# Kernel tuning notes

Measured on AMD Instinct MI355X. Metric: run time of the kernel, lower is better.

Reference implementation:

```python
import jax, jax.numpy as jnp
import numpy as np

# Bernstein-basis theta coefficients for d=2 (calculate_theta2(2)),
# inv_coeff order: [x^0, x^1, x^2]
THETAS = ((3.0, -3.0, 0.75), (0.0, 3.0, -1.5), (0.0, 0.0, 0.75))
HIGH_ORDER = 2

N_NODES = 50000
N_EDGES = 800000
IN_DIM, HID_DIM, OUT_DIM = 128, 64, 2


def setup_inputs() -> dict:
    key = jax.random.key(0)
    ks = jax.random.split(key, 16)
    f32 = jnp.float32
    def w(k, shape, fan_in):
        return jax.random.normal(k, shape, dtype=f32) * (1.0 / np.sqrt(fan_in))
    return {
        "in_feat": jax.random.normal(ks[0], (N_NODES, IN_DIM), dtype=f32),
        "src": jax.random.randint(ks[1], (N_EDGES,), 0, N_NODES, dtype=jnp.int32),
        "dst": jax.random.randint(ks[2], (N_EDGES,), 0, N_NODES, dtype=jnp.int32),
        "W1": w(ks[3], (IN_DIM, HID_DIM), IN_DIM), "b1": jnp.zeros((HID_DIM,), f32),
        "W2": w(ks[4], (HID_DIM, HID_DIM), HID_DIM), "b2": jnp.zeros((HID_DIM,), f32),
        "W3": w(ks[5], (HID_DIM * 5, HID_DIM), HID_DIM * 5), "b3": jnp.zeros((HID_DIM,), f32),
        "W4": w(ks[6], (HID_DIM, OUT_DIM), HID_DIM), "b4": jnp.zeros((OUT_DIM,), f32),
        "Wg1": w(ks[7], (IN_DIM, HID_DIM), IN_DIM), "bg1": jnp.zeros((HID_DIM,), f32),
        "Wg2": w(ks[8], (HID_DIM, IN_DIM), HID_DIM), "bg2": jnp.zeros((IN_DIM,), f32),
    }


def _spmm(x, src, dst, n):
    # y[v] = sum_{(u,v) in E} x[u]   (DGL update_all(copy_u, sum))
    return jax.ops.segment_sum(x[src], dst, num_segments=n)


def reference(in_feat, src, dst, W1, b1, W2, b2, W3, b3, W4, b4, Wg1, bg1, Wg2, bg2):
    n = in_feat.shape[0]
    ones_e = jnp.ones(src.shape[0], dtype=in_feat.dtype)
    deg_in = jnp.clip(jax.ops.segment_sum(ones_e, dst, num_segments=n), 1.0)
    deg_out = jnp.clip(jax.ops.segment_sum(ones_e, src, num_segments=n), 1.0)
    din = (deg_in ** -0.5)[:, None]   # [N,1]
    dout = (deg_out ** -0.5)[:, None]

    def lap(f):
        # f - D^{-1/2} A D^{-1/2} f  (in-degree norm, as in unnLaplacian)
        return f - _spmm(f * din, src, dst, n) * din

    # MLP front-end
    h = jax.nn.relu(in_feat @ W1 + b1)
    h = jax.nn.relu(h @ W2 + b2)

    branches = []
    # BandConv branches (lin=False): theta-weighted Laplacian polynomial
    for theta in THETAS:
        f = h
        acc = theta[0] * h
        for k in range(1, len(theta)):
            f = lap(f)
            acc = acc + theta[k] * f
        branches.append(acc)
    # HighConv branches: repeated Laplacian, num_layer = 1..HIGH_ORDER
    f = h
    for j in range(HIGH_ORDER):
        f = lap(f)
        branches.append(f)

    h_final = jnp.concatenate(branches, axis=-1)  # [N, 5*hid]
    out = jax.nn.relu(h_final @ W3 + b3) @ W4 + b4  # [N, out_dim]

    # GCN branch on self-loop-free graph (same edges here): symmetric norm GraphConv
    def gconv(x, W, b):
        return _spmm(x * dout, src, dst, n) * din @ W + b
    emb = gconv(jax.nn.relu(gconv(in_feat, Wg1, bg1)), Wg2, bg2)  # [N, in_dim]

    return out, emb
```

## Files before the change

kernel.cpp:

```cpp
#include <hip/hip_runtime.h>
#include <hip/hip_bf16.h>
#include <math.h>

#define NN 50000
#define NE 800000
#define C64 64
#define CE 12500
#define RW2 6250
#define NW 25000
#define HISTB 256
#define RB 98
#define GB 782
#define ZSB 782
#define FSG 3125
#define FSB 6250

typedef _Float16 half8 __attribute__((ext_vector_type(8)));
typedef _Float16 half4v __attribute__((ext_vector_type(4)));
typedef float f32x4 __attribute__((ext_vector_type(4)));
typedef unsigned short ushort4v __attribute__((ext_vector_type(4)));

static inline int cdiv(int a, int b) { return (a + b - 1) / b; }


__device__ inline size_t pack_pos(int k, int n, int K, int M) {
    int tile = n >> 4;
    int kstep = k >> 5;
    int quad = (k >> 3) & 3;
    int j = k & 7;
    int lane = (quad << 4) | (n & 15);
    return ((size_t)(tile * (K >> 5) + kstep) * 64 + lane) * 8 + j;
}

__device__ void pack_std_dev(int bx, const float* __restrict__ W, _Float16* __restrict__ Wpk,
                             int K, int M) {
    int idx = bx * 256 + threadIdx.x;
    if (idx >= K * M) return;
    int k = idx / M, n = idx % M;
    Wpk[pack_pos(k, n, K, M)] = (_Float16)W[idx];
}

__device__ void pack_wc_dev(int bx, const float* __restrict__ W3, _Float16* __restrict__ wcpk) {
    int idx = bx * 256 + threadIdx.x;
    if (idx >= 3 * 4096) return;
    int b = idx >> 12;
    int rem = idx & 4095;
    int k = rem >> 6, n = rem & 63;
    float w0 = W3[(0 * 64 + k) * 64 + n];
    float w1 = W3[(1 * 64 + k) * 64 + n];
    float w2 = W3[(2 * 64 + k) * 64 + n];
    float w3 = W3[(3 * 64 + k) * 64 + n];
    float w4 = W3[(4 * 64 + k) * 64 + n];
    float v;
    if (b == 0)      v = 3.f * w0;
    else if (b == 1) v = -3.f * w0 + 3.f * w1 + w3;
    else             v = 0.75f * w0 - 1.5f * w1 + 0.75f * w2 + w4;
    wcpk[pack_pos(b * 64 + k, n, 192, 64)] = (_Float16)v;
}

__launch_bounds__(256)
__global__ void k_init(const float* __restrict__ W1, _Float16* __restrict__ W1pk,
                       const float* __restrict__ W2, _Float16* __restrict__ W2pk,
                       const float* __restrict__ Wg1, _Float16* __restrict__ Wg1pk,
                       const float* __restrict__ Wg2, _Float16* __restrict__ Wg2pk,
                       const float* __restrict__ W3, _Float16* __restrict__ wcpk) {
    int bx = blockIdx.x;
    if (bx < 32) { pack_std_dev(bx, W1, W1pk, 128, 64); return; }
    bx -= 32;
    if (bx < 16) { pack_std_dev(bx, W2, W2pk, 64, 64); return; }
    bx -= 16;
    if (bx < 32) { pack_std_dev(bx, Wg1, Wg1pk, 128, 64); return; }
    bx -= 32;
    if (bx < 32) { pack_std_dev(bx, Wg2, Wg2pk, 64, 128); return; }
    bx -= 32;
    pack_wc_dev(bx, W3, wcpk);
}


__device__ void hist_dev(int bx, const int* __restrict__ idx, unsigned* __restrict__ H,
                         unsigned* __restrict__ cnt) {
    int c = bx & 63, r = bx >> 6;
    int tid = threadIdx.x;
    for (int j = tid; j < RW2; j += 256) cnt[j] = 0;
    __syncthreads();
    int lo = r * 12500;
    const int* p = idx + c * CE;
    for (int i = tid; i < CE; i += 256) {
        int v = p[i] - lo;
        if ((unsigned)v < 12500u)
            atomicAdd(&cnt[v >> 1], 1u << ((v & 1) * 16));
    }
    __syncthreads();
    unsigned* outp = H + (size_t)c * NW + r * RW2;
    for (int j = tid; j < RW2; j += 256) outp[j] = cnt[j];
}

__device__ void reduce_dev(int bx, const unsigned* __restrict__ H, int* __restrict__ dgo,
                           float* __restrict__ o_rsq, float* __restrict__ o_inv,
                           float* __restrict__ o_sq) {
    int w = bx * 256 + threadIdx.x;
    if (w >= NW) return;
    unsigned slo = 0, shi = 0;
#pragma unroll 8
    for (int c = 0; c < 64; c++) {
        unsigned h = H[(size_t)c * NW + w];
        slo += h & 0xffffu; shi += h >> 16;
    }
    if (dgo) {
        dgo[2 * w]     = slo > 64u ? 64 : (int)slo;
        dgo[2 * w + 1] = shi > 64u ? 64 : (int)shi;
    }
    float f0 = (float)(slo < 1u ? 1u : slo);
    float f1 = (float)(shi < 1u ? 1u : shi);
    o_rsq[2 * w] = rsqrtf(f0); o_rsq[2 * w + 1] = rsqrtf(f1);
    if (o_inv) { o_inv[2 * w] = 1.f / f0; o_inv[2 * w + 1] = 1.f / f1; }
    if (o_sq)  { o_sq[2 * w] = sqrtf(f0); o_sq[2 * w + 1] = sqrtf(f1); }
}

__device__ void prefix_dev(int bx, const unsigned* __restrict__ HD, unsigned* __restrict__ baseD) {
    int w = bx * 256 + threadIdx.x;
    if (w >= NW) return;
    unsigned slo = 0, shi = 0;
    for (int c = 0; c < 64; c++) {
        unsigned b0 = slo > 64u ? 64u : slo;
        unsigned b1 = shi > 64u ? 64u : shi;
        baseD[(size_t)c * NW + w] = b0 | (b1 << 16);
        unsigned h = HD[(size_t)c * NW + w];
        slo += h & 0xffffu; shi += h >> 16;
    }
}

__device__ void scatter_dev(int bx, const int* __restrict__ src, const int* __restrict__ dst,
                            const unsigned* __restrict__ baseD,
                            unsigned short* __restrict__ colsPad,
                            unsigned* __restrict__ cnt) {
    int c = bx & 63, r = bx >> 6;
    int tid = threadIdx.x;
    const unsigned* bslice = baseD + (size_t)c * NW + r * RW2;
    for (int j = tid; j < RW2; j += 256) cnt[j] = bslice[j];
    __syncthreads();
    int lo = r * 12500;
    const int* pd = dst + c * CE;
    const int* ps = src + c * CE;
    for (int i = tid; i < CE; i += 256) {
        int v = pd[i];
        int lv = v - lo;
        if ((unsigned)lv < 12500u) {
            int sh = (lv & 1) * 16;
            unsigned old = atomicAdd(&cnt[lv >> 1], 1u << sh);
            unsigned pos = (old >> sh) & 0xffffu;
            if (pos < 64u) colsPad[(size_t)v * 64 + pos] = (unsigned short)ps[i];
        }
    }
}

__device__ void zscale_dev(int bx, half8* __restrict__ zh8, const float* __restrict__ dout, int N) {
    int idx = bx * 256 + threadIdx.x;
    if (idx >= N * 4) return;
    int row = idx >> 2;
    float m = dout[row];
    half8 a = zh8[idx * 2], b = zh8[idx * 2 + 1];
#pragma unroll
    for (int j = 0; j < 8; j++) {
        a[j] = (_Float16)((float)a[j] * m);
        b[j] = (_Float16)((float)b[j] * m);
    }
    zh8[idx * 2] = a; zh8[idx * 2 + 1] = b;
}


struct HSegs { const _Float16* p[3]; int ld[3]; };

template <int M, int K, bool OUTW, bool RSCA>
__device__ void mg_dev(int bx, HSegs A, const half8* __restrict__ Wpk,
                       const float* __restrict__ bias, int relu,
                       float* __restrict__ C,
                       _Float16* __restrict__ Ch0, const float* __restrict__ ms0,
                       const float* __restrict__ rsc,
                       const float* __restrict__ W4, const float* __restrict__ b4,
                       float* __restrict__ outp, int N) {
    constexpr int NT = M / 16;
    constexpr int NKS = K / 32;
    int tid = threadIdx.x;
    int wave = tid >> 6, lane = tid & 63;
    int quad = lane >> 4, m = lane & 15;
    int row0 = bx * 64 + wave * 16;
    int rowA = row0 + m; if (rowA >= N) rowA = N - 1;
    _Float16 hs = (_Float16)1.f;
    if (RSCA) hs = (_Float16)rsc[rowA];
    f32x4 acc[NT];
#pragma unroll
    for (int t = 0; t < NT; t++) acc[t] = (f32x4){0.f, 0.f, 0.f, 0.f};
#pragma unroll
    for (int ks = 0; ks < NKS; ks++) {
        const _Float16* ap = A.p[ks >> 1] + (size_t)rowA * A.ld[ks >> 1] + (ks & 1) * 32 + quad * 8;
        half8 af = *(const half8*)ap;
        if (RSCA) {
#pragma unroll
            for (int j = 0; j < 8; j++) af[j] *= hs;
        }
#pragma unroll
        for (int t = 0; t < NT; t++) {
            half8 bf = Wpk[(t * NKS + ks) * 64 + lane];
            acc[t] = __builtin_amdgcn_mfma_f32_16x16x32_f16(af, bf, acc[t], 0, 0, 0);
        }
    }
    float outv[NT][4];
#pragma unroll
    for (int t = 0; t < NT; t++) {
        float bv = bias ? bias[t * 16 + m] : 0.f;
#pragma unroll
        for (int r = 0; r < 4; r++) {
            float v = acc[t][r] + bv;
            if (relu) v = fmaxf(v, 0.f);
            outv[t][r] = v;
        }
    }
    if (OUTW) {
        float w40[NT], w41[NT];
#pragma unroll
        for (int t = 0; t < NT; t++) {
            w40[t] = W4[(t * 16 + m) * 2];
            w41[t] = W4[(t * 16 + m) * 2 + 1];
        }
#pragma unroll
        for (int r = 0; r < 4; r++) {
            float p0 = 0.f, p1 = 0.f;
#pragma unroll
            for (int t = 0; t < NT; t++) {
                p0 += outv[t][r] * w40[t];
                p1 += outv[t][r] * w41[t];
            }
#pragma unroll
            for (int off = 1; off < 16; off <<= 1) {
                p0 += __shfl_xor(p0, off);
                p1 += __shfl_xor(p1, off);
            }
            int row = row0 + quad * 4 + r;
            if (m == 0 && row < N) {
                outp[(size_t)row * 2 + 0] = p0 + b4[0];
                outp[(size_t)row * 2 + 1] = p1 + b4[1];
            }
        }
    }
    if (C || Ch0) {
#pragma unroll
        for (int r = 0; r < 4; r++) {
            int row = row0 + quad * 4 + r;
            if (row >= N) continue;
            float m0 = (Ch0 && ms0) ? ms0[row] : 1.f;
#pragma unroll
            for (int t = 0; t < NT; t++) {
                size_t off = (size_t)row * M + t * 16 + m;
                if (C)   C[off] = outv[t][r];
                if (Ch0) Ch0[off] = (_Float16)(outv[t][r] * m0);
            }
        }
    }
}

__device__ void a15_dev(int bx, const float* __restrict__ in_feat,
                        const half8* __restrict__ W1pk, const half8* __restrict__ Wg1pk,
                        const float* __restrict__ b1,
                        _Float16* __restrict__ h1h, _Float16* __restrict__ zh, int N) {
    int tid = threadIdx.x;
    int wave = tid >> 6, lane = tid & 63;
    int quad = lane >> 4, m = lane & 15;
    int row0 = bx * 64 + wave * 16;
    int rowA = row0 + m; if (rowA >= N) rowA = N - 1;
    f32x4 acc0[4], acc1[4];
#pragma unroll
    for (int t = 0; t < 4; t++) {
        acc0[t] = (f32x4){0.f, 0.f, 0.f, 0.f};
        acc1[t] = (f32x4){0.f, 0.f, 0.f, 0.f};
    }
#pragma unroll
    for (int ks = 0; ks < 4; ks++) {
        const float* ap = in_feat + (size_t)rowA * 128 + ks * 32 + quad * 8;
        float4 u = *(const float4*)ap;
        float4 v = *(const float4*)(ap + 4);
        half8 af;
        af[0] = (_Float16)u.x; af[1] = (_Float16)u.y; af[2] = (_Float16)u.z; af[3] = (_Float16)u.w;
        af[4] = (_Float16)v.x; af[5] = (_Float16)v.y; af[6] = (_Float16)v.z; af[7] = (_Float16)v.w;
#pragma unroll
        for (int t = 0; t < 4; t++) {
            acc0[t] = __builtin_amdgcn_mfma_f32_16x16x32_f16(af, W1pk[(t * 4 + ks) * 64 + lane], acc0[t], 0, 0, 0);
            acc1[t] = __builtin_amdgcn_mfma_f32_16x16x32_f16(af, Wg1pk[(t * 4 + ks) * 64 + lane], acc1[t], 0, 0, 0);
        }
    }
#pragma unroll
    for (int r = 0; r < 4; r++) {
        int row = row0 + quad * 4 + r;
        if (row >= N) continue;
#pragma unroll
        for (int t = 0; t < 4; t++) {
            float v0 = fmaxf(acc0[t][r] + b1[t * 16 + m], 0.f);
            h1h[(size_t)row * 64 + t * 16 + m] = (_Float16)v0;
            zh[(size_t)row * 64 + t * 16 + m] = (_Float16)acc1[t][r];
        }
    }
}


__launch_bounds__(256)
__global__ void k_L1(const int* __restrict__ src, const int* __restrict__ dst,
                     unsigned* __restrict__ HD, unsigned* __restrict__ HS,
                     const float* __restrict__ in_feat,
                     const half8* __restrict__ W1pk, const half8* __restrict__ Wg1pk,
                     const float* __restrict__ b1,
                     _Float16* __restrict__ h1h, _Float16* __restrict__ zh, int N) {
    __shared__ unsigned cnt[RW2];
    int bx = blockIdx.x;
    if (bx < HISTB) { hist_dev(bx, dst, HD, cnt); return; }
    bx -= HISTB;
    if (bx < HISTB) { hist_dev(bx, src, HS, cnt); return; }
    bx -= HISTB;
    a15_dev(bx, in_feat, W1pk, Wg1pk, b1, h1h, zh, N);
}

__launch_bounds__(256)
__global__ void k_L2(const unsigned* __restrict__ HD, const unsigned* __restrict__ HS,
                     int* __restrict__ degin, float* __restrict__ din,
                     float* __restrict__ din2, float* __restrict__ dsq,
                     float* __restrict__ dout, unsigned* __restrict__ baseD) {
    int bx = blockIdx.x;
    if (bx < RB) { reduce_dev(bx, HD, degin, din, din2, dsq); return; }
    bx -= RB;
    if (bx < RB) { reduce_dev(bx, HS, nullptr, dout, nullptr, nullptr); return; }
    bx -= RB;
    prefix_dev(bx, HD, baseD);
}

__launch_bounds__(256)
__global__ void k_L3(const int* __restrict__ src, const int* __restrict__ dst,
                     const unsigned* __restrict__ baseD, unsigned short* __restrict__ colsPad,
                     const _Float16* __restrict__ h1h, const half8* __restrict__ W2pk,
                     const float* __restrict__ b2, _Float16* __restrict__ u0h,
                     const float* __restrict__ din,
                     half8* __restrict__ zh8, const float* __restrict__ dout, int N) {
    __shared__ unsigned cnt[RW2];
    int bx = blockIdx.x;
    if (bx < HISTB) { scatter_dev(bx, src, dst, baseD, colsPad, cnt); return; }
    bx -= HISTB;
    if (bx < GB) {
        HSegs A;
        A.p[0] = h1h; A.ld[0] = 64;
        A.p[1] = nullptr; A.ld[1] = 0;
        A.p[2] = nullptr; A.ld[2] = 0;
        mg_dev<64, 64, false, false>(bx, A, W2pk, b2, 1, nullptr, u0h, din,
                                     nullptr, nullptr, nullptr, nullptr, N);
        return;
    }
    bx -= GB;
    zscale_dev(bx, zh8, dout, N);
}


struct SpmmP {
    const half4v* xh; const half4v* fsub_h; const float* rowscale; const float* bias;
    half4v* yh0; const float* ms0; int relu;
};

__launch_bounds__(256)
__global__ void k_FS(SpmmP P0, SpmmP P1, const unsigned short* __restrict__ colsPad,
                     const int* __restrict__ deg, int N) {
    int bx = blockIdx.x;
    bool first = bx < FSG;
    SpmmP P = first ? P0 : P1;
    int g = first ? bx : bx - FSG;
    int tid = threadIdx.x;
    int wave = tid >> 6, lane = tid & 63;
    int quad = lane >> 4, c = lane & 15;
    int row = g * 16 + wave * 4 + quad;
    if (row >= N) return;
    int dg = deg[row];
    const unsigned short* cp = colsPad + (size_t)row * 64;
    float ax = 0.f, ay = 0.f, az = 0.f, aw = 0.f;
    int e = 0;
    for (; e + 7 < dg; e += 8) {
        ushort4v sa = *(const ushort4v*)(cp + e);
        ushort4v sb = *(const ushort4v*)(cp + e + 4);
        half4v v0 = P.xh[(size_t)sa.x * 16 + c];
        half4v v1 = P.xh[(size_t)sa.y * 16 + c];
        half4v v2 = P.xh[(size_t)sa.z * 16 + c];
        half4v v3 = P.xh[(size_t)sa.w * 16 + c];
        half4v v4 = P.xh[(size_t)sb.x * 16 + c];
        half4v v5 = P.xh[(size_t)sb.y * 16 + c];
        half4v v6 = P.xh[(size_t)sb.z * 16 + c];
        half4v v7 = P.xh[(size_t)sb.w * 16 + c];
        ax += (float)v0.x + (float)v1.x + (float)v2.x + (float)v3.x
            + (float)v4.x + (float)v5.x + (float)v6.x + (float)v7.x;
        ay += (float)v0.y + (float)v1.y + (float)v2.y + (float)v3.y
            + (float)v4.y + (float)v5.y + (float)v6.y + (float)v7.y;
        az += (float)v0.z + (float)v1.z + (float)v2.z + (float)v3.z
            + (float)v4.z + (float)v5.z + (float)v6.z + (float)v7.z;
        aw += (float)v0.w + (float)v1.w + (float)v2.w + (float)v3.w
            + (float)v4.w + (float)v5.w + (float)v6.w + (float)v7.w;
    }
    for (; e + 3 < dg; e += 4) {
        ushort4v ss = *(const ushort4v*)(cp + e);
        half4v v0 = P.xh[(size_t)ss.x * 16 + c];
        half4v v1 = P.xh[(size_t)ss.y * 16 + c];
        half4v v2 = P.xh[(size_t)ss.z * 16 + c];
        half4v v3 = P.xh[(size_t)ss.w * 16 + c];
        ax += (float)v0.x + (float)v1.x + (float)v2.x + (float)v3.x;
        ay += (float)v0.y + (float)v1.y + (float)v2.y + (float)v3.y;
        az += (float)v0.z + (float)v1.z + (float)v2.z + (float)v3.z;
        aw += (float)v0.w + (float)v1.w + (float)v2.w + (float)v3.w;
    }
    for (; e < dg; e++) {
        int s = cp[e];
        half4v v = P.xh[(size_t)s * 16 + c];
        ax += (float)v.x; ay += (float)v.y; az += (float)v.z; aw += (float)v.w;
    }
    size_t oidx = (size_t)row * 16 + c;
    if (P.fsub_h) {
        float d = P.rowscale[row];
        half4v f = P.fsub_h[oidx];
        ax = (float)f.x - ax * d; ay = (float)f.y - ay * d;
        az = (float)f.z - az * d; aw = (float)f.w - aw * d;
    } else {
        if (P.rowscale) { float d = P.rowscale[row]; ax *= d; ay *= d; az *= d; aw *= d; }
        if (P.bias) {
            float4 bb = ((const float4*)P.bias)[c];
            ax += bb.x; ay += bb.y; az += bb.z; aw += bb.w;
        }
        if (P.relu) {
            ax = fmaxf(ax, 0.f); ay = fmaxf(ay, 0.f);
            az = fmaxf(az, 0.f); aw = fmaxf(aw, 0.f);
        }
    }
    float mm = P.ms0 ? P.ms0[row] : 1.f;
    half4v h;
    h.x = (_Float16)(ax * mm); h.y = (_Float16)(ay * mm);
    h.z = (_Float16)(az * mm); h.w = (_Float16)(aw * mm);
    P.yh0[oidx] = h;
}

__launch_bounds__(256)
__global__ void k_F3(const _Float16* __restrict__ u0h, const _Float16* __restrict__ u1h,
                     const _Float16* __restrict__ u2h, const half8* __restrict__ wcpk,
                     const float* __restrict__ b3, const float* __restrict__ dsq,
                     const float* __restrict__ W4, const float* __restrict__ b4,
                     float* __restrict__ outp,
                     const _Float16* __restrict__ sgh, const half8* __restrict__ Wg2pk,
                     const float* __restrict__ bg2, float* __restrict__ emb, int N) {
    int bx = blockIdx.x;
    if (bx < GB) {
        HSegs A;
        A.p[0] = u0h; A.ld[0] = 64;
        A.p[1] = u1h; A.ld[1] = 64;
        A.p[2] = u2h; A.ld[2] = 64;
        mg_dev<64, 192, true, true>(bx, A, wcpk, b3, 1, nullptr, nullptr, nullptr,
                                    dsq, W4, b4, outp, N);
        return;
    }
    bx -= GB;
    HSegs A;
    A.p[0] = sgh; A.ld[0] = 64;
    A.p[1] = nullptr; A.ld[1] = 0;
    A.p[2] = nullptr; A.ld[2] = 0;
    mg_dev<128, 64, false, false>(bx, A, Wg2pk, bg2, 0, emb, nullptr, nullptr,
                                  nullptr, nullptr, nullptr, nullptr, N);
}

extern "C" void kernel_launch(void* const* d_in, const int* in_sizes, int n_in,
                              void* d_out, int out_size, void* d_ws, size_t ws_size,
                              hipStream_t stream) {
    const int N = NN;
    const float* in_feat = (const float*)d_in[0];
    const int* src = (const int*)d_in[1];
    const int* dst = (const int*)d_in[2];
    const float* W1 = (const float*)d_in[3];
    const float* b1 = (const float*)d_in[4];
    const float* W2 = (const float*)d_in[5];
    const float* b2 = (const float*)d_in[6];
    const float* W3 = (const float*)d_in[7];
    const float* b3 = (const float*)d_in[8];
    const float* W4 = (const float*)d_in[9];
    const float* b4 = (const float*)d_in[10];
    const float* Wg1 = (const float*)d_in[11];
    const float* bg1 = (const float*)d_in[12];
    const float* Wg2 = (const float*)d_in[13];
    const float* bg2 = (const float*)d_in[14];

    float* out = (float*)d_out;
    float* emb = out + (size_t)N * 2;

    float* fw = (float*)d_ws;
    float* din  = fw;
    float* din2 = din + N;
    float* dsq  = din2 + N;
    float* dout = dsq + N;
    int* degin  = (int*)(dout + N);
    unsigned short* colsPad = (unsigned short*)(degin + N);
    unsigned* HD   = (unsigned*)(colsPad + (size_t)64 * N);
    unsigned* HS   = HD + (size_t)C64 * NW;
    unsigned* baseD = HS + (size_t)C64 * NW;
    _Float16* hp = (_Float16*)(baseD + (size_t)C64 * NW);
    _Float16* h1h   = hp;
    _Float16* u0h   = h1h + (size_t)64 * N;
    _Float16* u1h   = u0h + (size_t)64 * N;
    _Float16* u2h   = u1h + (size_t)64 * N;
    _Float16* zh    = u2h + (size_t)64 * N;
    _Float16* g1h   = zh + (size_t)64 * N;
    _Float16* sgh   = g1h + (size_t)64 * N;
    _Float16* W1pk  = sgh + (size_t)64 * N;
    _Float16* W2pk  = W1pk + 8192;
    _Float16* Wg1pk = W2pk + 4096;
    _Float16* Wg2pk = Wg1pk + 8192;
    _Float16* wcpk  = Wg2pk + 8192;

    k_init<<<160, 256, 0, stream>>>(W1, W1pk, W2, W2pk, Wg1, Wg1pk, Wg2, Wg2pk, W3, wcpk);

    k_L1<<<2 * HISTB + GB, 256, 0, stream>>>(src, dst, HD, HS, in_feat,
        (const half8*)W1pk, (const half8*)Wg1pk, b1, h1h, zh, N);

    k_L2<<<2 * RB + RB, 256, 0, stream>>>(HD, HS, degin, din, din2, dsq, dout, baseD);

    k_L3<<<HISTB + GB + ZSB, 256, 0, stream>>>(src, dst, baseD, colsPad,
        h1h, (const half8*)W2pk, b2, u0h, din, (half8*)zh, dout, N);

    SpmmP p0, p1;
    p0 = {(const half4v*)u0h, (const half4v*)u0h, din2, nullptr, (half4v*)u1h, nullptr, 0};
    p1 = {(const half4v*)zh, nullptr, din, bg1, (half4v*)g1h, dout, 1};
    k_FS<<<FSB, 256, 0, stream>>>(p0, p1, colsPad, degin, N);

    p0 = {(const half4v*)u1h, (const half4v*)u1h, din2, nullptr, (half4v*)u2h, nullptr, 0};
    p1 = {(const half4v*)g1h, nullptr, nullptr, nullptr, (half4v*)sgh, din, 0};
    k_FS<<<FSB, 256, 0, stream>>>(p0, p1, colsPad, degin, N);

    k_F3<<<2 * GB, 256, 0, stream>>>(u0h, u1h, u2h, (const half8*)wcpk, b3, dsq,
        W4, b4, out, sgh, (const half8*)Wg2pk, bg2, emb, N);
}
```

Baseline: 260.2 us.

## Merge weight packing into histogram launch and halve histogram chunk count

Folds the weight-packing kernel into the first launch alongside the degree histograms, and moves the first dense GEMM (a15) into the second launch next to the reduce/prefix blocks. This drops one kernel launch and its inter-kernel gap. The edge list is now split into 32 chunks instead of 64, so each histogram and scatter block handles twice as many edges and the per-chunk count arrays written, reduced and prefix-scanned are half as large. The cost is fewer, longer histogram blocks with less parallelism. The GEMM also now waits behind the histogram stage instead of overlapping with it.

```diff
diff --git a/kernel.cpp b/kernel.cpp
--- a/kernel.cpp
+++ b/kernel.cpp
@@ -4,11 +4,12 @@
 
 #define NN 50000
 #define NE 800000
-#define C64 64
-#define CE 12500
+#define C32 32
+#define CE 25000
 #define RW2 6250
 #define NW 25000
-#define HISTB 256
+#define HISTB 128
+#define INITB 160
 #define RB 98
 #define GB 782
 #define ZSB 782
@@ -58,13 +59,12 @@
     wcpk[pack_pos(b * 64 + k, n, 192, 64)] = (_Float16)v;
 }
 
-__launch_bounds__(256)
-__global__ void k_init(const float* __restrict__ W1, _Float16* __restrict__ W1pk,
-                       const float* __restrict__ W2, _Float16* __restrict__ W2pk,
-                       const float* __restrict__ Wg1, _Float16* __restrict__ Wg1pk,
-                       const float* __restrict__ Wg2, _Float16* __restrict__ Wg2pk,
-                       const float* __restrict__ W3, _Float16* __restrict__ wcpk) {
-    int bx = blockIdx.x;
+__device__ void init_dev(int bx,
+                         const float* __restrict__ W1, _Float16* __restrict__ W1pk,
+                         const float* __restrict__ W2, _Float16* __restrict__ W2pk,
+                         const float* __restrict__ Wg1, _Float16* __restrict__ Wg1pk,
+                         const float* __restrict__ Wg2, _Float16* __restrict__ Wg2pk,
+                         const float* __restrict__ W3, _Float16* __restrict__ wcpk) {
     if (bx < 32) { pack_std_dev(bx, W1, W1pk, 128, 64); return; }
     bx -= 32;
     if (bx < 16) { pack_std_dev(bx, W2, W2pk, 64, 64); return; }
@@ -79,12 +79,12 @@
 
 __device__ void hist_dev(int bx, const int* __restrict__ idx, unsigned* __restrict__ H,
                          unsigned* __restrict__ cnt) {
-    int c = bx & 63, r = bx >> 6;
+    int c = bx & 31, r = bx >> 5;
     int tid = threadIdx.x;
     for (int j = tid; j < RW2; j += 256) cnt[j] = 0;
     __syncthreads();
     int lo = r * 12500;
-    const int* p = idx + c * CE;
+    const int* p = idx + (size_t)c * CE;
     for (int i = tid; i < CE; i += 256) {
         int v = p[i] - lo;
         if ((unsigned)v < 12500u)
@@ -102,7 +102,7 @@
     if (w >= NW) return;
     unsigned slo = 0, shi = 0;
 #pragma unroll 8
-    for (int c = 0; c < 64; c++) {
+    for (int c = 0; c < C32; c++) {
         unsigned h = H[(size_t)c * NW + w];
         slo += h & 0xffffu; shi += h >> 16;
     }
@@ -121,7 +121,7 @@
     int w = bx * 256 + threadIdx.x;
     if (w >= NW) return;
     unsigned slo = 0, shi = 0;
-    for (int c = 0; c < 64; c++) {
+    for (int c = 0; c < C32; c++) {
         unsigned b0 = slo > 64u ? 64u : slo;
         unsigned b1 = shi > 64u ? 64u : shi;
         baseD[(size_t)c * NW + w] = b0 | (b1 << 16);
@@ -134,14 +134,14 @@
                             const unsigned* __restrict__ baseD,
                             unsigned short* __restrict__ colsPad,
                             unsigned* __restrict__ cnt) {
-    int c = bx & 63, r = bx >> 6;
+    int c = bx & 31, r = bx >> 5;
     int tid = threadIdx.x;
     const unsigned* bslice = baseD + (size_t)c * NW + r * RW2;
     for (int j = tid; j < RW2; j += 256) cnt[j] = bslice[j];
     __syncthreads();
     int lo = r * 12500;
-    const int* pd = dst + c * CE;
-    const int* ps = src + c * CE;
+    const int* pd = dst + (size_t)c * CE;
+    const int* ps = src + (size_t)c * CE;
     for (int i = tid; i < CE; i += 256) {
         int v = pd[i];
         int lv = v - lo;
@@ -303,32 +303,39 @@
 
 
 __launch_bounds__(256)
-__global__ void k_L1(const int* __restrict__ src, const int* __restrict__ dst,
-                     unsigned* __restrict__ HD, unsigned* __restrict__ HS,
+__global__ void k_L1(const float* __restrict__ W1, _Float16* __restrict__ W1pk,
+                     const float* __restrict__ W2, _Float16* __restrict__ W2pk,
+                     const float* __restrict__ Wg1, _Float16* __restrict__ Wg1pk,
+                     const float* __restrict__ Wg2, _Float16* __restrict__ Wg2pk,
+                     const float* __restrict__ W3, _Float16* __restrict__ wcpk,
+                     const int* __restrict__ src, const int* __restrict__ dst,
+                     unsigned* __restrict__ HD, unsigned* __restrict__ HS) {
+    __shared__ unsigned cnt[RW2];
+    int bx = blockIdx.x;
+    if (bx < INITB) { init_dev(bx, W1, W1pk, W2, W2pk, Wg1, Wg1pk, Wg2, Wg2pk, W3, wcpk); return; }
+    bx -= INITB;
+    if (bx < HISTB) { hist_dev(bx, dst, HD, cnt); return; }
+    bx -= HISTB;
+    hist_dev(bx, src, HS, cnt);
+}
+
+__launch_bounds__(256)
+__global__ void k_L2(const unsigned* __restrict__ HD, const unsigned* __restrict__ HS,
+                     int* __restrict__ degin, float* __restrict__ din,
+                     float* __restrict__ din2, float* __restrict__ dsq,
+                     float* __restrict__ dout, unsigned* __restrict__ baseD,
                      const float* __restrict__ in_feat,
                      const half8* __restrict__ W1pk, const half8* __restrict__ Wg1pk,
                      const float* __restrict__ b1,
                      _Float16* __restrict__ h1h, _Float16* __restrict__ zh, int N) {
-    __shared__ unsigned cnt[RW2];
-    int bx = blockIdx.x;
-    if (bx < HISTB) { hist_dev(bx, dst, HD, cnt); return; }
-    bx -= HISTB;
-    if (bx < HISTB) { hist_dev(bx, src, HS, cnt); return; }
-    bx -= HISTB;
-    a15_dev(bx, in_feat, W1pk, Wg1pk, b1, h1h, zh, N);
-}
-
-__launch_bounds__(256)
-__global__ void k_L2(const unsigned* __restrict__ HD, const unsigned* __restrict__ HS,
-                     int* __restrict__ degin, float* __restrict__ din,
-                     float* __restrict__ din2, float* __restrict__ dsq,
-                     float* __restrict__ dout, unsigned* __restrict__ baseD) {
     int bx = blockIdx.x;
     if (bx < RB) { reduce_dev(bx, HD, degin, din, din2, dsq); return; }
     bx -= RB;
     if (bx < RB) { reduce_dev(bx, HS, nullptr, dout, nullptr, nullptr); return; }
     bx -= RB;
-    prefix_dev(bx, HD, baseD);
+    if (bx < RB) { prefix_dev(bx, HD, baseD); return; }
+    bx -= RB;
+    a15_dev(bx, in_feat, W1pk, Wg1pk, b1, h1h, zh, N);
 }
 
 __launch_bounds__(256)
@@ -495,9 +502,9 @@
     int* degin  = (int*)(dout + N);
     unsigned short* colsPad = (unsigned short*)(degin + N);
     unsigned* HD   = (unsigned*)(colsPad + (size_t)64 * N);
-    unsigned* HS   = HD + (size_t)C64 * NW;
-    unsigned* baseD = HS + (size_t)C64 * NW;
-    _Float16* hp = (_Float16*)(baseD + (size_t)C64 * NW);
+    unsigned* HS   = HD + (size_t)C32 * NW;
+    unsigned* baseD = HS + (size_t)C32 * NW;
+    _Float16* hp = (_Float16*)(baseD + (size_t)C32 * NW);
     _Float16* h1h   = hp;
     _Float16* u0h   = h1h + (size_t)64 * N;
     _Float16* u1h   = u0h + (size_t)64 * N;
@@ -511,12 +518,11 @@
     _Float16* Wg2pk = Wg1pk + 8192;
     _Float16* wcpk  = Wg2pk + 8192;
 
-    k_init<<<160, 256, 0, stream>>>(W1, W1pk, W2, W2pk, Wg1, Wg1pk, Wg2, Wg2pk, W3, wcpk);
-
-    k_L1<<<2 * HISTB + GB, 256, 0, stream>>>(src, dst, HD, HS, in_feat,
-        (const half8*)W1pk, (const half8*)Wg1pk, b1, h1h, zh, N);
-
-    k_L2<<<2 * RB + RB, 256, 0, stream>>>(HD, HS, degin, din, din2, dsq, dout, baseD);
+    k_L1<<<INITB + 2 * HISTB, 256, 0, stream>>>(W1, W1pk, W2, W2pk, Wg1, Wg1pk,
+        Wg2, Wg2pk, W3, wcpk, src, dst, HD, HS);
+
+    k_L2<<<3 * RB + GB, 256, 0, stream>>>(HD, HS, degin, din, din2, dsq, dout, baseD,
+        in_feat, (const half8*)W1pk, (const half8*)Wg1pk, b1, h1h, zh, N);
 
     k_L3<<<HISTB + GB + ZSB, 256, 0, stream>>>(src, dst, baseD, colsPad,
         h1h, (const half8*)W2pk, b2, u0h, din, (half8*)zh, dout, N);
```

Result: slower. 293.9 us (+13.0%).
